# Optimization experiments

Hardware: AMD Instinct MI355X
Metric: run time of the kernel (lower is better)

## Reference

```python
import jax, jax.numpy as jnp
import numpy as np

V = 27578   # super-model vertex count (self.shape)
NJ = 24     # joints
NB = 10     # shape PCA coeffs
NP = (NJ - 1) * 9  # 207 pose-blend features
K = 24000   # kept vertices (to_keep)
B = 32
# standard SMPL kinematic tree: PARENTS[i] is the parent joint of joint i (i>=1)
PARENTS = np.array([0, 0, 0, 0, 1, 2, 3, 4, 5, 6, 7, 8, 9, 9, 9, 12, 13, 14, 16, 17, 18, 19, 20, 21], dtype=np.int32)


def setup_inputs() -> dict:
    key = jax.random.key(0)
    ks = jax.random.split(key, 8)
    pose = jax.random.normal(ks[0], (B, NJ, 3), dtype=jnp.float32) * 0.4
    betas = jax.random.normal(ks[1], (B, NB + 1), dtype=jnp.float32)  # last entry = gender flag
    J_regressor = jax.random.uniform(ks[2], (2, NJ, V), dtype=jnp.float32)
    J_regressor = J_regressor / jnp.sum(J_regressor, axis=-1, keepdims=True)
    v_template = jax.random.normal(ks[3], (2, V, 3), dtype=jnp.float32)
    shapedirs = jax.random.normal(ks[4], (2, V, 3, NB), dtype=jnp.float32) * 0.03
    posedirs = jax.random.normal(ks[5], (2, V, 3, NP), dtype=jnp.float32) * 0.01
    weights_all = jax.random.uniform(ks[6], (2, V, NJ), dtype=jnp.float32)
    weights_all = weights_all / jnp.sum(weights_all, axis=-1, keepdims=True)
    to_keep = jnp.sort(jax.random.randint(ks[7], (K,), 0, V, dtype=jnp.int32))
    return {"pose": pose, "betas": betas, "J_regressor": J_regressor,
            "v_template": v_template, "shapedirs": shapedirs, "posedirs": posedirs,
            "weights_all": weights_all, "to_keep": to_keep}


def rodrigues(r):
    """Axis-angle [N,3] -> rotation matrices [N,3,3] (Rodrigues formula)."""
    eps = jnp.float32(np.finfo(np.float32).eps)
    theta = jnp.maximum(jnp.linalg.norm(r, axis=-1, keepdims=True), eps)  # [N,1]
    rh = r / theta
    z = jnp.zeros_like(rh[:, 0])
    m = jnp.stack([z, -rh[:, 2], rh[:, 1],
                   rh[:, 2], z, -rh[:, 0],
                   -rh[:, 1], rh[:, 0], z], axis=1).reshape(-1, 3, 3)
    t = theta[:, :, None]  # [N,1,1]
    I = jnp.eye(3, dtype=r.dtype)
    return I + m * jnp.sin(t) + jnp.matmul(m, m) * (1.0 - jnp.cos(t))


def reference(pose, betas, J_regressor, v_template, shapedirs, posedirs, weights_all, to_keep):
    b = betas.shape[0]
    dt = pose.dtype
    g = betas[:, -1] > 0.5  # gender: True -> male (index 1)
    sel = lambda f, m: jnp.where(g[:, None, None], m, f)

    # shape blendshapes for both genders, select per sample
    vs_f = jnp.einsum('bs,vcs->bvc', betas[:, :NB], shapedirs[0]) + v_template[0]
    vs_m = jnp.einsum('bs,vcs->bvc', betas[:, :NB], shapedirs[1]) + v_template[1]

    J_f = jnp.einsum('jv,bvc->bjc', J_regressor[0], vs_f)
    J_m = jnp.einsum('jv,bvc->bjc', J_regressor[1], vs_m)
    J = sel(J_f, J_m)  # [b,24,3]

    # Rodrigues per joint
    R = rodrigues(pose.reshape(-1, 3)).reshape(b, NJ, 3, 3)

    # pose blendshapes
    lrot = (R[:, 1:] - jnp.eye(3, dtype=dt)).reshape(b, NP)  # [b,207]
    off_f = jnp.einsum('bp,vcp->bvc', lrot, posedirs[0])
    off_m = jnp.einsum('bp,vcp->bvc', lrot, posedirs[1])
    v_posed = sel(vs_f, vs_m) + sel(off_f, off_m)  # [b,V,3]

    # local joint transforms [b,24,4,4]
    J_rel = jnp.concatenate([J[:, :1], J[:, 1:] - J[:, PARENTS[1:]]], axis=1)
    A = jnp.concatenate([R, J_rel[..., None]], axis=-1)  # [b,24,3,4]
    bottom = jnp.broadcast_to(jnp.array([0., 0., 0., 1.], dtype=dt), (b, NJ, 1, 4))
    A = jnp.concatenate([A, bottom], axis=2)

    # kinematic chain (sequential 24-joint tree)
    Gs = [A[:, 0]]
    for i in range(1, NJ):
        Gs.append(jnp.matmul(Gs[int(PARENTS[i])], A[:, i]))
    G = jnp.stack(Gs, axis=1)  # [b,24,4,4]

    # subtract rest-pose joint contribution: results = G - pack(G @ [J;0])
    Jh0 = jnp.concatenate([J, jnp.zeros((b, NJ, 1), dtype=dt)], axis=-1)
    corr = jnp.einsum('bjpq,bjq->bjp', G, Jh0)
    results = G.at[:, :, :, 3].add(-corr)

    Jh1 = jnp.concatenate([J, jnp.ones((b, NJ, 1), dtype=dt)], axis=-1)
    joints = jnp.einsum('bjpq,bjq->bjp', results, Jh1)[:, :, :3]

    # linear blend skinning with gender-matched weights
    w = jnp.where(g[:, None, None], weights_all[1][None], weights_all[0][None])  # [b,V,24]
    T = jnp.einsum('bjpq,bvj->bvpq', results, w)  # [b,V,4,4]
    vh = jnp.concatenate([v_posed, jnp.ones((b, V, 1), dtype=dt)], axis=-1)
    v = jnp.einsum('bvpq,bvq->bvp', T, vh)[:, :, :3]

    root = joints[:, :1]
    result = (v - root)[:, to_keep, :]  # [b,K,3]
    return result
```

## Files before the change

### kernel.cpp

```cpp
#include <hip/hip_runtime.h>
#include <hip/hip_bf16.h>
#include <cstdint>
#include <cstddef>

#define V      27578
#define NJ     24
#define KK     24000
#define NT2    1724
#define NCHUNK 25
#define VCHUNK 1104

#define LPD    0
#define LA     12288
#define LRB    16000
#define LVP    24192
#define LT     26368
#define LWA    36608
#define LTM2   37120
#define LROOT2 37216
#define LPERM2 37312
#define LCNT2  37344
#define LKB    37348
#define LDSW   37364

#define WS_JS   0
#define WS_LA   39600
#define WS_RB   43312
#define WS_ROOT 51824
#define WS_PERM 51920
#define WS_CNT  51952
#define WS_KB   51956

typedef short short8 __attribute__((ext_vector_type(8)));
typedef float f32x4 __attribute__((ext_vector_type(4)));

union S8U4 { unsigned u[4]; uint4 u4; short8 s; };

__device__ __forceinline__ unsigned pk2(float a, float b) {
    __hip_bfloat162 h = __float22bfloat162_rn(float2{a, b});
    union { __hip_bfloat162 h; unsigned u; } cv; cv.h = h;
    return cv.u;
}

__constant__ int d_par[24] = {0,0,0,0,1,2,3,4,5,6,7,8,9,9,9,12,13,14,16,17,18,19,20,21};

__global__ __launch_bounds__(256) void k_js(const float* __restrict__ jreg,
                                            const float* __restrict__ vtmpl,
                                            const float* __restrict__ sdirs,
                                            float* __restrict__ ws) {
    const int chunk = blockIdx.x, jg = blockIdx.y, g = blockIdx.z;
    const int tid = threadIdx.x;
    float acc[4][33];
#pragma unroll
    for (int a = 0; a < 4; ++a)
#pragma unroll
        for (int o = 0; o < 33; ++o) acc[a][o] = 0.f;

    const int v0 = chunk * VCHUNK;
    const int v1 = (v0 + VCHUNK < V) ? v0 + VCHUNK : V;
    const float* jr0 = jreg + (size_t)g * NJ * V;
    const float* sd  = sdirs + (size_t)g * V * 30;
    const float* tm  = vtmpl + (size_t)g * V * 3;

    for (int v = v0 + tid; v < v1; v += 256) {
        float jv[4];
#pragma unroll
        for (int a = 0; a < 4; ++a) jv[a] = jr0[(size_t)(jg*4 + a) * V + v];
        float b[33];
        const float* sdv = sd + (size_t)v * 30;
#pragma unroll
        for (int o = 0; o < 30; o += 2) {
            float2 q = *(const float2*)(sdv + o);
            b[o] = q.x; b[o+1] = q.y;
        }
        b[30] = tm[(size_t)v*3 + 0];
        b[31] = tm[(size_t)v*3 + 1];
        b[32] = tm[(size_t)v*3 + 2];
#pragma unroll
        for (int a = 0; a < 4; ++a)
#pragma unroll
            for (int o = 0; o < 33; ++o) acc[a][o] += jv[a] * b[o];
    }

#pragma unroll
    for (int a = 0; a < 4; ++a)
#pragma unroll
        for (int o = 0; o < 33; ++o) {
            float x = acc[a][o];
#pragma unroll
            for (int s = 32; s >= 1; s >>= 1) x += __shfl_xor(x, s, 64);
            acc[a][o] = x;
        }

    __shared__ float red[4][132];
    const int wvi = tid >> 6, ln = tid & 63;
    if (ln == 0) {
#pragma unroll
        for (int a = 0; a < 4; ++a)
#pragma unroll
            for (int o = 0; o < 33; ++o) red[wvi][a*33 + o] = acc[a][o];
    }
    __syncthreads();
    if (tid < 132) {
        float s = red[0][tid] + red[1][tid] + red[2][tid] + red[3][tid];
        int a = tid / 33, o = tid % 33;
        int j = jg * 4 + a;
        ws[(size_t)((g*NJ + j)*33 + o) * NCHUNK + chunk] = s;
    }
}

__global__ __launch_bounds__(256) void k_joint(const float* __restrict__ pose,
                                               const float* __restrict__ betas,
                                               const int*   __restrict__ to_keep,
                                               float* __restrict__ ws) {
    const int bid = (int)blockIdx.x;
    const int t = threadIdx.x;
    int* wsI = (int*)ws;
    unsigned* wsU = (unsigned*)ws;

    if (bid >= 32) {
        int idx = (bid - 32) * 256 + t;
        if (idx <= NT2) {
            int target = idx * 16;
            int lo = 0, hi = KK;
            while (lo < hi) { int m = (lo + hi) >> 1; if (to_keep[m] < target) lo = m + 1; else hi = m; }
            wsI[WS_KB + idx] = lo;
        }
        return;
    }

    __shared__ float gflag[32];
    __shared__ int   permJ[33];
    __shared__ float jsJ[792];
    __shared__ float Jloc[96];
    __shared__ float AJ[288];
    __shared__ float GS[288];

    if (t < 32) gflag[t] = betas[t*11 + 10];
    __syncthreads();
    if (t < 32) {
        bool male = gflag[t] > 0.5f;
        unsigned gm = (unsigned)__ballot(male);
        int cnt0 = 32 - __popc(gm);
        unsigned below = (1u << t) - 1u;
        int slot = male ? (cnt0 + __popc(gm & below)) : __popc((~gm) & below);
        permJ[slot] = t;
        if (t == 0) permJ[32] = cnt0;
    }
    __syncthreads();

    const int slot = bid;
    const int b = permJ[slot];
    const int gi = (gflag[b] > 0.5f) ? 1 : 0;

    if (bid == 0) {
        if (t < 32) wsI[WS_PERM + t] = permJ[t];
        if (t == 0) wsI[WS_CNT] = permJ[32];
    }

    for (int o = t; o < 792; o += 256) {
        const float* p = ws + WS_JS + (size_t)(gi*792 + o) * NCHUNK;
        float s = 0.f;
#pragma unroll
        for (int c = 0; c < NCHUNK; ++c) s += p[c];
        jsJ[o] = s;
    }
    __syncthreads();

    if (t < 72) {
        int j = t / 3, c = t - 3*j;
        const float* jsb = jsJ + j*33;
        float s = jsb[30 + c];
#pragma unroll
        for (int q = 0; q < 10; ++q) s += jsb[c*10 + q] * betas[b*11 + q];
        Jloc[j*4 + c] = s;
    }
    __syncthreads();

    if (t < 24) {
        const float* pp = pose + (size_t)(b*24 + t) * 3;
        float rx = pp[0], ry = pp[1], rz = pp[2];
        float th = fmaxf(sqrtf(rx*rx + ry*ry + rz*rz), 1.1920929e-07f);
        float inv = 1.0f / th;
        float ux = rx*inv, uy = ry*inv, uz = rz*inv;
        float st = sinf(th), ct = cosf(th), oc = 1.0f - ct;
        float* A = AJ + t*12;
        A[0] = ct + oc*ux*ux;    A[1] = oc*ux*uy - st*uz; A[2]  = oc*ux*uz + st*uy;
        A[4] = oc*ux*uy + st*uz; A[5] = ct + oc*uy*uy;    A[6]  = oc*uy*uz - st*ux;
        A[8] = oc*ux*uz - st*uy; A[9] = oc*uy*uz + st*ux; A[10] = ct + oc*uz*uz;
        int par = d_par[t];
#pragma unroll
        for (int r = 0; r < 3; ++r)
            A[r*4 + 3] = Jloc[t*4 + r] - (t > 0 ? Jloc[par*4 + r] : 0.f);
    }
    __syncthreads();

    if (t < 116) {
        float f[2];
#pragma unroll
        for (int h = 0; h < 2; ++h) {
            int k = 2*t + h;
            float val = 0.f;
            if (k < 207) {
                int j = k / 9 + 1, rc = k - 9*(j-1);
                int r = rc / 3, c = rc - 3*r;
                val = AJ[j*12 + r*4 + c] - (r == c ? 1.f : 0.f);
            } else if (k >= 208 && k < 218) {
                val = betas[b*11 + (k - 208)];
            }
            f[h] = val;
        }
        wsU[WS_LA + slot*116 + t] = pk2(f[0], f[1]);
    }

    if (t < 12) {
        constexpr int kPar[24] = {0,0,0,0,1,2,3,4,5,6,7,8,9,9,9,12,13,14,16,17,18,19,20,21};
        const int r = t >> 2, c = t & 3;
        float Greg[24];
        Greg[0] = AJ[t];
#pragma unroll
        for (int j = 1; j < 24; ++j) {
            const int par = kPar[j];
            float a0 = AJ[j*12 + 0 + c];
            float a1 = AJ[j*12 + 4 + c];
            float a2 = AJ[j*12 + 8 + c];
            float g0 = __shfl(Greg[par], r*4 + 0, 64);
            float g1 = __shfl(Greg[par], r*4 + 1, 64);
            float g2 = __shfl(Greg[par], r*4 + 2, 64);
            float g3 = __shfl(Greg[par], r*4 + 3, 64);
            Greg[j] = g0*a0 + g1*a1 + g2*a2 + (c == 3 ? g3 : 0.f);
        }
#pragma unroll
        for (int j = 0; j < 24; ++j) {
            float t0 = __shfl(Greg[j], r*4 + 0, 64);
            float t1 = __shfl(Greg[j], r*4 + 1, 64);
            float t2 = __shfl(Greg[j], r*4 + 2, 64);
            float corr = t0*Jloc[j*4 + 0] + t1*Jloc[j*4 + 1] + t2*Jloc[j*4 + 2];
            if (c == 3) Greg[j] -= corr;
            GS[j*12 + t] = Greg[j];
        }
    }
    __syncthreads();

    {
        int kg = t >> 6, rem = t & 63, n = rem >> 2, wq = rem & 3;
        int j0 = kg*8 + 2*wq;
        float f0 = (j0 < 24 && n < 12) ? GS[j0*12 + n] : 0.f;
        float f1 = (j0 + 1 < 24 && n < 12) ? GS[(j0+1)*12 + n] : 0.f;
        wsU[WS_RB + slot*256 + t] = pk2(f0, f1);
    }
    if (t < 3) {
        float s = GS[t*4 + 3];
#pragma unroll
        for (int q = 0; q < 3; ++q) s += GS[t*4 + q] * Jloc[q];
        ws[WS_ROOT + slot*3 + t] = s;
    }
}

__global__ __launch_bounds__(1024) void k_pose(const float* __restrict__ posedirs,
                                               const float* __restrict__ sdirs,
                                               const float* __restrict__ vtmpl,
                                               const float* __restrict__ wall,
                                               const int*   __restrict__ to_keep,
                                               const float* __restrict__ ws,
                                               float* __restrict__ out) {
    extern __shared__ float L[];
    unsigned* Lu = (unsigned*)L;
    int* Li = (int*)L;
    const unsigned* wsU = (const unsigned*)ws;
    const int* wsI = (const int*)ws;
    const int t = threadIdx.x;
    const int l = t & 63, wv = t >> 6;
    const int lm = l & 15, lg = l >> 4;
    const int bid = (int)blockIdx.x;

    int pdoff[5], pdladr[5];
    bool pdok[5], pdq3[5];
#pragma unroll
    for (int n = 0; n < 5; ++n) {
        int e = t + 1024*n;
        bool ok = e < 4992;
        pdok[n] = ok;
        int e2 = ok ? e : 0;
        int row = e2 / 52, k4 = (e2 - 52*row) * 4;
        int g = row / 48, rr = row - 48*g;
        pdoff[n] = g*(V*621) + rr*207 + k4;
        int kw = k4 >> 1;
        pdladr[n] = LPD + row*128 + (kw ^ ((row & 7) << 2));
        pdq3[n] = (k4 == 204);
    }
    int sdoff = 0, sdladr = 0;
    if (t < 480) {
        int w = 2*t;
        int g = w / 480, w2 = w - 480*g;
        int row = w2 / 10, j = (w2 - 10*row) >> 1;
        int rowg = g*48 + row;
        sdoff = g*(V*30) + w2;
        sdladr = LPD + rowg*128 + ((104 + j) ^ ((rowg & 7) << 2));
    }
    int tmoff = 0;
    if (t < 48)  { int w = 2*t; int g = w/48;  tmoff = g*(V*3) + (w - 48*g); }
    int woff = 0, wladr = 0;
    if (t < 384) {
        int g = t/192, i = t - 192*g;
        int v = i/12, wi = i - 12*v;
        int kgrp = wi >> 2, wq = wi & 3;
        int j0 = kgrp*8 + 2*wq;
        woff = g*(V*24) + v*24 + j0;
        wladr = LWA + g*256 + kgrp*64 + v*4 + wq;
    }

    float4 pdreg[5]; float2 sdreg = {0,0}, tmreg = {0,0}, wreg = {0,0};

    const int PDLIM = 2*V*621 - 4;
    const int SDLIM = 2*V*30 - 2;
    const int TMLIM = 2*V*3 - 2;
    const int WLIM  = 2*V*24 - 2;

    auto issue_loads = [&](int itm) {
        const int vb = itm * 16;
#pragma unroll
        for (int n = 0; n < 5; ++n) {
            int a = vb*621 + pdoff[n];
            if (a > PDLIM) a = PDLIM;
            pdreg[n].x = posedirs[a];
            pdreg[n].y = posedirs[a+1];
            pdreg[n].z = posedirs[a+2];
            pdreg[n].w = pdq3[n] ? 0.f : posedirs[a+3];
        }
        if (t < 480) { int a = vb*30 + sdoff; if (a > SDLIM) a = SDLIM; sdreg = *(const float2*)(sdirs + a); }
        if (t < 48)  { int a = vb*3  + tmoff; if (a > TMLIM) a = TMLIM; tmreg = *(const float2*)(vtmpl + a); }
        if (t < 384) { int a = vb*24 + woff;  if (a > WLIM)  a = WLIM;  wreg  = *(const float2*)(wall  + a); }
    };

    auto write_stage = [&]() {
#pragma unroll
        for (int n = 0; n < 5; ++n)
            if (pdok[n]) {
                uint2 v;
                v.x = pk2(pdreg[n].x, pdreg[n].y);
                v.y = pk2(pdreg[n].z, pdreg[n].w);
                *(uint2*)&Lu[pdladr[n]] = v;
            }
        if (t < 480) Lu[sdladr] = pk2(sdreg.x, sdreg.y);
        if (t < 48)  { L[LTM2 + 2*t] = tmreg.x; L[LTM2 + 2*t + 1] = tmreg.y; }
        if (t < 384) Lu[wladr] = pk2(wreg.x, wreg.y);
    };

    issue_loads(bid);

    {
        for (int i = t; i < 928; i += 1024)
            *(uint4*)&Lu[LA + 4*i] = *(const uint4*)&wsU[WS_LA + 4*i];
        for (int i = t; i < 2048; i += 1024)
            *(uint4*)&Lu[LRB + 4*i] = *(const uint4*)&wsU[WS_RB + 4*i];
        if (t < 96)  L[LROOT2 + t] = ws[WS_ROOT + t];
        if (t < 32)  Li[LPERM2 + t] = wsI[WS_PERM + t];
        if (t == 0)  Li[LCNT2] = wsI[WS_CNT];
        if (t < 8) {
            int idx = bid + 256*t;
            int kst = KK, ken = KK;
            if (idx < NT2) { kst = wsI[WS_KB + idx]; ken = wsI[WS_KB + idx + 1]; }
            Li[LKB + t] = kst; Li[LKB + 8 + t] = ken;
        }
        if (t < 128) Lu[LWA + (t >> 6)*256 + 192 + (t & 63)] = 0;
        if (t < 288) {
            int row = t / 3, j2 = 109 + (t - 3*(t/3));
            Lu[LPD + row*128 + (j2 ^ ((row & 7) << 2))] = 0;
        }
        __syncthreads();
    }

    const int cnt0v = Li[LCNT2];
    const int cnt1 = 32 - cnt0v;
    const int m0 = (cnt0v + 15) >> 4, m1 = (cnt1 + 15) >> 4;
    const int ntA = 3*m0, ntasks = 3*(m0 + m1);

    int rb0 = -1, nt0 = 0, sb0 = 0, ct0 = 0, gi0 = 0;
    if (wv < ntasks) {
        int gi = (wv >= ntA) ? 1 : 0; int tt = gi ? wv - ntA : wv;
        int mt = tt / 3; nt0 = tt - 3*mt;
        sb0 = gi ? cnt0v : 0; ct0 = gi ? cnt1 : cnt0v;
        rb0 = sb0 + mt*16; gi0 = gi;
    }

    const int bs = t >> 5, kl0 = t & 31;
    const int borig = Li[LPERM2 + bs];
    const float rt0 = L[LROOT2 + bs*3 + 0];
    const float rt1 = L[LROOT2 + bs*3 + 1];
    const float rt2 = L[LROOT2 + bs*3 + 2];
    const int s4 = (lm & 7) << 2;

    write_stage();
    __syncthreads();

    int li = 0;
    for (int item = bid; item < NT2; item += 256, ++li) {
        const bool more = (item + 256 < NT2);
        if (more) issue_loads(item + 256);

        f32x4 acc0 = {0,0,0,0};
        if (rb0 >= 0) {
            const unsigned* ap = Lu + LA + (rb0 + lm)*116 + (lg << 2);
            const unsigned* bp = Lu + LPD + (gi0*48 + nt0*16 + lm)*128;
#pragma unroll
            for (int kk = 0; kk < 7; ++kk) {
                S8U4 a; a.u4 = *(const uint4*)(ap + kk*16);
                S8U4 bb; bb.u4 = *(const uint4*)(bp + ((kk*16 + (lg << 2)) ^ s4));
                acc0 = __builtin_amdgcn_mfma_f32_16x16x32_bf16(a.s, bb.s, acc0, 0, 0, 0);
            }
        }

        if (rb0 >= 0) {
            int n = nt0*16 + lm;
            int vd = n / 3, cd = n - 3*vd;
            float tmv = L[LTM2 + gi0*48 + n];
#pragma unroll
            for (int r = 0; r < 4; ++r) {
                int slot = rb0 + (lg << 2) + r;
                if ((unsigned)(slot - sb0) < (unsigned)ct0)
                    L[LVP + slot*68 + vd*4 + cd] = acc0[r] + tmv;
            }
        }

#pragma unroll
        for (int q = 0; q < 2; ++q) {
            int s = wv*2 + q;
            int gsl = (s >= cnt0v) ? 1 : 0;
            S8U4 a; a.u4 = *(const uint4*)(Lu + LWA + gsl*256 + lg*64 + lm*4);
            S8U4 b; b.u4 = *(const uint4*)(Lu + LRB + s*256 + lg*64 + lm*4);
            f32x4 acT = {0,0,0,0};
            acT = __builtin_amdgcn_mfma_f32_16x16x32_bf16(a.s, b.s, acT, 0, 0, 0);
#pragma unroll
            for (int r = 0; r < 4; ++r)
                L[LT + s*320 + (lg*4 + r)*20 + lm] = acT[r];
        }
        __syncthreads();

        const int kst = Li[LKB + li], ken = Li[LKB + 8 + li];
        const int v0w = item * 16;
        for (int k = kst + kl0; k < ken; k += 32) {
            const int vr = to_keep[k] - v0w;
            const float4 vp = *(const float4*)&L[LVP + bs*68 + vr*4];
            const float4 t0 = *(const float4*)&L[LT + bs*320 + vr*20];
            const float4 t1 = *(const float4*)&L[LT + bs*320 + vr*20 + 4];
            const float4 t2 = *(const float4*)&L[LT + bs*320 + vr*20 + 8];
            const size_t ob = ((size_t)borig*KK + (size_t)k)*3;
            out[ob]   = t0.x*vp.x + t0.y*vp.y + t0.z*vp.z + t0.w - rt0;
            out[ob+1] = t1.x*vp.x + t1.y*vp.y + t1.z*vp.z + t1.w - rt1;
            out[ob+2] = t2.x*vp.x + t2.y*vp.y + t2.z*vp.z + t2.w - rt2;
        }
        if (more) write_stage();
        __syncthreads();
    }
}

extern "C" void kernel_launch(void* const* d_in, const int* in_sizes, int n_in,
                              void* d_out, int out_size, void* d_ws, size_t ws_size,
                              hipStream_t stream) {
    const float* pose     = (const float*)d_in[0];
    const float* betas    = (const float*)d_in[1];
    const float* jreg     = (const float*)d_in[2];
    const float* vtmpl    = (const float*)d_in[3];
    const float* sdirs    = (const float*)d_in[4];
    const float* posedirs = (const float*)d_in[5];
    const float* wall     = (const float*)d_in[6];
    const int*   to_keep  = (const int*)d_in[7];
    float* ws  = (float*)d_ws;
    float* out = (float*)d_out;

    hipFuncSetAttribute((const void*)k_pose,
                        hipFuncAttributeMaxDynamicSharedMemorySize,
                        LDSW * 4);

    hipLaunchKernelGGL(k_js,    dim3(NCHUNK, 6, 2), dim3(256), 0, stream, jreg, vtmpl, sdirs, ws);
    hipLaunchKernelGGL(k_joint, dim3(40),           dim3(256), 0, stream, pose, betas, to_keep, ws);
    hipLaunchKernelGGL(k_pose,  dim3(256),          dim3(1024), LDSW * 4, stream,
                       posedirs, sdirs, vtmpl, wall, to_keep, ws, out);
}
```

Baseline: 81.93 us.

## Coalesce posedirs staging loads and tile shapedirs through LDS in joint regressor

The pose kernel now loads posedirs as contiguous float2 pairs across the flat 16-vertex slab. It scatters the individual bf16 halves into the swizzled LDS layout through precomputed packed half-word addresses, replacing the scalar strided per-row loads. Separately, k_js stages shapedirs and template rows into a shared tile with float4 coalesced loads before the per-vertex FMA, instead of reading strided rows per thread. The aim is to reduce uncoalesced global traffic, at the cost of more LDS writes, extra syncs, and 16-bit LDS stores that may cause bank conflicts.

```diff
diff --git a/kernel.cpp b/kernel.cpp
--- a/kernel.cpp
+++ b/kernel.cpp
@@ -9,6 +9,7 @@
 #define NT2    1724
 #define NCHUNK 25
 #define VCHUNK 1104
+#define VW     17125938
 
 #define LPD    0
 #define LA     12288
@@ -42,6 +43,12 @@
     return cv.u;
 }
 
+__device__ __forceinline__ unsigned short bf16b(float x) {
+    union { __hip_bfloat16 h; unsigned short u; } c;
+    c.h = __float2bfloat16(x);
+    return c.u;
+}
+
 __constant__ int d_par[24] = {0,0,0,0,1,2,3,4,5,6,7,8,9,9,9,12,13,14,16,17,18,19,20,21};
 
 __global__ __launch_bounds__(256) void k_js(const float* __restrict__ jreg,
@@ -50,6 +57,9 @@
                                             float* __restrict__ ws) {
     const int chunk = blockIdx.x, jg = blockIdx.y, g = blockIdx.z;
     const int tid = threadIdx.x;
+    __shared__ float tile[256 * 33];
+    __shared__ float red[4][132];
+
     float acc[4][33];
 #pragma unroll
     for (int a = 0; a < 4; ++a)
@@ -62,24 +72,39 @@
     const float* sd  = sdirs + (size_t)g * V * 30;
     const float* tm  = vtmpl + (size_t)g * V * 3;
 
-    for (int v = v0 + tid; v < v1; v += 256) {
-        float jv[4];
-#pragma unroll
-        for (int a = 0; a < 4; ++a) jv[a] = jr0[(size_t)(jg*4 + a) * V + v];
-        float b[33];
-        const float* sdv = sd + (size_t)v * 30;
-#pragma unroll
-        for (int o = 0; o < 30; o += 2) {
-            float2 q = *(const float2*)(sdv + o);
-            b[o] = q.x; b[o+1] = q.y;
-        }
-        b[30] = tm[(size_t)v*3 + 0];
-        b[31] = tm[(size_t)v*3 + 1];
-        b[32] = tm[(size_t)v*3 + 2];
-#pragma unroll
-        for (int a = 0; a < 4; ++a)
-#pragma unroll
-            for (int o = 0; o < 33; ++o) acc[a][o] += jv[a] * b[o];
+    for (int vt = v0; vt < v1; vt += 256) {
+        const int cnt = (v1 - vt < 256) ? (v1 - vt) : 256;
+        const float* sb = sd + (size_t)vt * 30;
+        const int nf4 = (cnt * 30) >> 2;
+        for (int i4 = tid; i4 < nf4; i4 += 256) {
+            float4 q = *(const float4*)(sb + 4 * i4);
+            int w = 4 * i4;
+#pragma unroll
+            for (int e = 0; e < 4; ++e) {
+                int w2 = w + e;
+                int dv = w2 / 30, o = w2 - 30 * dv;
+                float val = (e == 0) ? q.x : (e == 1) ? q.y : (e == 2) ? q.z : q.w;
+                tile[dv * 33 + o] = val;
+            }
+        }
+        const float* tb = tm + (size_t)vt * 3;
+        for (int i = tid; i < cnt * 3; i += 256) {
+            int dv = i / 3, c = i - 3 * dv;
+            tile[dv * 33 + 30 + c] = tb[i];
+        }
+        __syncthreads();
+        if (tid < cnt) {
+            const int v = vt + tid;
+            float jv[4];
+#pragma unroll
+            for (int a = 0; a < 4; ++a) jv[a] = jr0[(size_t)(jg*4 + a) * V + v];
+            const float* bb = tile + tid * 33;
+#pragma unroll
+            for (int a = 0; a < 4; ++a)
+#pragma unroll
+                for (int o = 0; o < 33; ++o) acc[a][o] += jv[a] * bb[o];
+        }
+        __syncthreads();
     }
 
 #pragma unroll
@@ -92,7 +117,6 @@
             acc[a][o] = x;
         }
 
-    __shared__ float red[4][132];
     const int wvi = tid >> 6, ln = tid & 63;
     if (ln == 0) {
 #pragma unroll
@@ -266,6 +290,7 @@
                                                float* __restrict__ out) {
     extern __shared__ float L[];
     unsigned* Lu = (unsigned*)L;
+    unsigned short* Lh = (unsigned short*)L;
     int* Li = (int*)L;
     const unsigned* wsU = (const unsigned*)ws;
     const int* wsI = (const int*)ws;
@@ -274,20 +299,26 @@
     const int lm = l & 15, lg = l >> 4;
     const int bid = (int)blockIdx.x;
 
-    int pdoff[5], pdladr[5];
-    bool pdok[5], pdq3[5];
-#pragma unroll
-    for (int n = 0; n < 5; ++n) {
-        int e = t + 1024*n;
-        bool ok = e < 4992;
-        pdok[n] = ok;
-        int e2 = ok ? e : 0;
-        int row = e2 / 52, k4 = (e2 - 52*row) * 4;
-        int g = row / 48, rr = row - 48*g;
-        pdoff[n] = g*(V*621) + rr*207 + k4;
-        int kw = k4 >> 1;
-        pdladr[n] = LPD + row*128 + (kw ^ ((row & 7) << 2));
-        pdq3[n] = (k4 == 204);
+    const bool pd9 = (t < 720);
+    unsigned pdba[10];
+#pragma unroll
+    for (int n = 0; n < 10; ++n) {
+        int f2 = t + 1024*n;
+        if (f2 >= 9936) f2 = 0;
+        int gsel = (f2 >= 4968) ? 1 : 0;
+        int off2 = 2*(f2 - 4968*gsel);
+        unsigned ba2 = 0;
+#pragma unroll
+        for (int e = 0; e < 2; ++e) {
+            int w = off2 + e;
+            int row = w / 207;
+            int k = w - 207*row;
+            int rowg = gsel*48 + row;
+            int word = LPD + rowg*128 + ((k >> 1) ^ ((rowg & 7) << 2));
+            unsigned hw = (unsigned)(word*2 + (k & 1));
+            ba2 |= hw << (16*e);
+        }
+        pdba[n] = ba2;
     }
     int sdoff = 0, sdladr = 0;
     if (t < 480) {
@@ -310,24 +341,24 @@
         wladr = LWA + g*256 + kgrp*64 + v*4 + wq;
     }
 
-    float4 pdreg[5]; float2 sdreg = {0,0}, tmreg = {0,0}, wreg = {0,0};
-
-    const int PDLIM = 2*V*621 - 4;
+    float2 pdreg[10];
+    float2 sdreg = {0,0}, tmreg = {0,0}, wreg = {0,0};
+
     const int SDLIM = 2*V*30 - 2;
     const int TMLIM = 2*V*3 - 2;
     const int WLIM  = 2*V*24 - 2;
 
     auto issue_loads = [&](int itm) {
+        const int base = itm * 9936;
+#pragma unroll
+        for (int n = 0; n < 10; ++n) {
+            if (n == 9 && !pd9) continue;
+            int f2 = t + 1024*n;
+            int w = base + 2*f2 + ((f2 >= 4968) ? (VW - 9936) : 0);
+            if (w > 2*VW - 2) w = 2*VW - 2;
+            pdreg[n] = *(const float2*)(posedirs + w);
+        }
         const int vb = itm * 16;
-#pragma unroll
-        for (int n = 0; n < 5; ++n) {
-            int a = vb*621 + pdoff[n];
-            if (a > PDLIM) a = PDLIM;
-            pdreg[n].x = posedirs[a];
-            pdreg[n].y = posedirs[a+1];
-            pdreg[n].z = posedirs[a+2];
-            pdreg[n].w = pdq3[n] ? 0.f : posedirs[a+3];
-        }
         if (t < 480) { int a = vb*30 + sdoff; if (a > SDLIM) a = SDLIM; sdreg = *(const float2*)(sdirs + a); }
         if (t < 48)  { int a = vb*3  + tmoff; if (a > TMLIM) a = TMLIM; tmreg = *(const float2*)(vtmpl + a); }
         if (t < 384) { int a = vb*24 + woff;  if (a > WLIM)  a = WLIM;  wreg  = *(const float2*)(wall  + a); }
@@ -335,13 +366,12 @@
 
     auto write_stage = [&]() {
 #pragma unroll
-        for (int n = 0; n < 5; ++n)
-            if (pdok[n]) {
-                uint2 v;
-                v.x = pk2(pdreg[n].x, pdreg[n].y);
-                v.y = pk2(pdreg[n].z, pdreg[n].w);
-                *(uint2*)&Lu[pdladr[n]] = v;
-            }
+        for (int n = 0; n < 10; ++n) {
+            if (n == 9 && !pd9) continue;
+            unsigned p = pdba[n];
+            Lh[p & 0xffffu] = bf16b(pdreg[n].x);
+            Lh[p >> 16]     = bf16b(pdreg[n].y);
+        }
         if (t < 480) Lu[sdladr] = pk2(sdreg.x, sdreg.y);
         if (t < 48)  { L[LTM2 + 2*t] = tmreg.x; L[LTM2 + 2*t + 1] = tmreg.y; }
         if (t < 384) Lu[wladr] = pk2(wreg.x, wreg.y);
@@ -364,6 +394,8 @@
             Li[LKB + t] = kst; Li[LKB + 8 + t] = ken;
         }
         if (t < 128) Lu[LWA + (t >> 6)*256 + 192 + (t & 63)] = 0;
+        if (t < 96)
+            Lu[LPD + t*128 + (103 ^ ((t & 7) << 2))] = 0;
         if (t < 288) {
             int row = t / 3, j2 = 109 + (t - 3*(t/3));
             Lu[LPD + row*128 + (j2 ^ ((row & 7) << 2))] = 0;
```

Result: slower. 114.3 us (+39.5%).
